# Performance work log

Measured on AMD Instinct MI355X. Metric: run time of the kernel, lower is better.

Reference implementation:

```python
import jax, jax.numpy as jnp
import numpy as np

N_NODES = 100000

def spmm(rows, cols, vals, x):
    # out[r] = sum_e vals[e] * x[cols[e]] for edges with rows[e] == r
    msgs = vals[:, None] * x[cols]            # [E, F]
    return jax.ops.segment_sum(msgs, rows, num_segments=N_NODES)

def setup_inputs() -> dict:
    key = jax.random.key(0)
    ks = jax.random.split(key, 8)
    N, E, F_IN, H, C = N_NODES, 1600000, 128, 128, 64
    x = jax.random.normal(ks[0], (N, F_IN), dtype=jnp.float32)
    edge_rows = jax.random.randint(ks[1], (E,), 0, N, dtype=jnp.int32)
    edge_cols = jax.random.randint(ks[2], (E,), 0, N, dtype=jnp.int32)
    edge_vals = jax.random.uniform(ks[3], (E,), dtype=jnp.float32)
    W1 = jax.random.normal(ks[4], (F_IN, H), dtype=jnp.float32) * (1.0 / np.sqrt(F_IN))
    b1 = jnp.zeros((H,), dtype=jnp.float32)
    W2 = jax.random.normal(ks[5], (H, C), dtype=jnp.float32) * (1.0 / np.sqrt(H))
    b2 = jnp.zeros((C,), dtype=jnp.float32)
    return {"x": x, "edge_rows": edge_rows, "edge_cols": edge_cols,
            "edge_vals": edge_vals, "W1": W1, "b1": b1, "W2": W2, "b2": b2}

def reference(x, edge_rows, edge_cols, edge_vals, W1, b1, W2, b2):
    # Layer 1: spmm(adj, x) then linear, then ReLU (dropout = identity at eval)
    h = spmm(edge_rows, edge_cols, edge_vals, x)   # [N, F_IN]
    h = h @ W1 + b1                                # [N, H]
    h = jax.nn.relu(h)
    # Layer 2
    h = spmm(edge_rows, edge_cols, edge_vals, h)   # [N, H]
    return h @ W2 + b2                             # [N, C]
```

## Files before the change

kernel.cpp:

```cpp
#include <hip/hip_runtime.h>


typedef __attribute__((ext_vector_type(8))) short short8;
typedef __attribute__((ext_vector_type(4))) float floatx4;
typedef __attribute__((ext_vector_type(2))) float floatx2;

#define ELLS 64
#define RW   256
#define CH   4096
#define EPT  16
#define MAXB 400

static __device__ __forceinline__ unsigned short f2bf(float f) {
    unsigned int u = __builtin_bit_cast(unsigned int, f);
    u += 0x7fffu + ((u >> 16) & 1u);
    return (unsigned short)(u >> 16);
}
static __device__ __forceinline__ float bflo(unsigned int u) {
    return __builtin_bit_cast(float, u << 16);
}
static __device__ __forceinline__ float bfhi(unsigned int u) {
    return __builtin_bit_cast(float, u & 0xffff0000u);
}
static __device__ __forceinline__ float slotval(unsigned int s) {
    return (float)(s >> 17) * (1.0f / 32767.0f);
}

__global__ __launch_bounds__(256) void prep_kernel(
    const float* __restrict__ W1, const float* __restrict__ W2,
    unsigned short* __restrict__ W1t, unsigned short* __restrict__ W2t)
{
    int idx = blockIdx.x * 256 + threadIdx.x;
    if (idx < 128 * 128) {
        int n = idx >> 7, k = idx & 127;
        W1t[idx] = f2bf(W1[(size_t)k * 128 + n]);
    }
    if (idx < 64 * 128) {
        int n = idx >> 7, k = idx & 127;
        W2t[idx] = f2bf(W2[(size_t)k * 64 + n]);
    }
}

static __device__ __forceinline__ void gemm1_body(
    const float* __restrict__ A, const unsigned short* __restrict__ Wt,
    unsigned short* __restrict__ Ys, int NP, int N, int bid)
{
    const int lane = threadIdx.x & 63;
    const int wave = threadIdx.x >> 6;
    const int quad = lane >> 4;
    const int l16  = lane & 15;
    const int row0 = bid * 64 + wave * 16;
    int arow = row0 + l16;
    if (arow > N - 1) arow = N - 1;

    short8 af[4];
    const float* ap = A + (size_t)arow * 128 + quad * 8;
    #pragma unroll
    for (int kt = 0; kt < 4; ++kt) {
        const floatx4* p = (const floatx4*)(ap + kt * 32);
        floatx4 lo = __builtin_nontemporal_load(p);
        floatx4 hi = __builtin_nontemporal_load(p + 1);
        short8 t;
        t[0] = (short)f2bf(lo[0]); t[1] = (short)f2bf(lo[1]);
        t[2] = (short)f2bf(lo[2]); t[3] = (short)f2bf(lo[3]);
        t[4] = (short)f2bf(hi[0]); t[5] = (short)f2bf(hi[1]);
        t[6] = (short)f2bf(hi[2]); t[7] = (short)f2bf(hi[3]);
        af[kt] = t;
    }

    floatx4 acc[8];
    #pragma unroll
    for (int nt = 0; nt < 8; ++nt) acc[nt] = (floatx4){0.f, 0.f, 0.f, 0.f};

    #pragma unroll
    for (int nt = 0; nt < 8; ++nt) {
        const unsigned short* wp = Wt + (size_t)(nt * 16 + l16) * 128 + quad * 8;
        #pragma unroll
        for (int kt = 0; kt < 4; ++kt) {
            short8 bfr = *(const short8*)(wp + kt * 32);
            acc[nt] = __builtin_amdgcn_mfma_f32_16x16x32_bf16(
                af[kt], bfr, acc[nt], 0, 0, 0);
        }
    }

    #pragma unroll
    for (int nt = 0; nt < 8; ++nt) {
        #pragma unroll
        for (int r = 0; r < 4; ++r) {
            int row = row0 + quad * 4 + r;
            if (row < N)
                Ys[(size_t)nt * NP * 16 + (size_t)row * 16 + l16] =
                    f2bf(acc[nt][r]);
        }
    }
}

__global__ __launch_bounds__(256) void binA_gemm1_fused(
    const int* __restrict__ erow, const int* __restrict__ ecol,
    const float* __restrict__ eval,
    uint2* __restrict__ slab, unsigned int* __restrict__ offsT,
    int E, int NC, int NB,
    const float* __restrict__ x, const unsigned short* __restrict__ W1t,
    unsigned short* __restrict__ y1s, int NP, int N)
{
    __shared__ unsigned int hist[MAXB + 1];
    __shared__ uint2 compact[CH];

    if ((int)blockIdx.x < NC) {
        const int t     = threadIdx.x;
        const int chunk = blockIdx.x;

        for (int i = t; i <= NB; i += 256) hist[i] = 0;
        __syncthreads();

        int base = chunk * CH + t * EPT;
        unsigned int w0[EPT];
        unsigned int vb[EPT];
        int bk[EPT], rk[EPT];

        if (base + EPT <= E) {
            #pragma unroll
            for (int q = 0; q < 4; ++q) {
                int4   r4 = *(const int4*)(erow + base + q * 4);
                int4   c4 = *(const int4*)(ecol + base + q * 4);
                float4 v4 = *(const float4*)(eval + base + q * 4);
                int rr[4]   = {r4.x, r4.y, r4.z, r4.w};
                int cc[4]   = {c4.x, c4.y, c4.z, c4.w};
                float vv[4] = {v4.x, v4.y, v4.z, v4.w};
                #pragma unroll
                for (int j = 0; j < 4; ++j) {
                    int i = q * 4 + j;
                    bk[i] = rr[j] >> 8;
                    w0[i] = (unsigned int)cc[j]
                          | (((unsigned int)rr[j] & (RW - 1)) << 17);
                    vb[i] = __builtin_bit_cast(unsigned int, vv[j]);
                }
            }
        } else {
            #pragma unroll
            for (int j = 0; j < EPT; ++j) {
                int e = base + j;
                if (e < E) {
                    int r = erow[e];
                    bk[j] = r >> 8;
                    w0[j] = (unsigned int)ecol[e]
                          | (((unsigned int)r & (RW - 1)) << 17);
                    vb[j] = __builtin_bit_cast(unsigned int, eval[e]);
                } else {
                    bk[j] = NB;
                    w0[j] = 0u; vb[j] = 0u;
                }
            }
        }

        #pragma unroll
        for (int j = 0; j < EPT; ++j)
            rk[j] = (int)atomicAdd(&hist[bk[j]], 1u);
        __syncthreads();

        if (t == 0) {
            unsigned int run = 0;
            for (int i = 0; i <= NB; ++i) {
                unsigned int c = hist[i];
                hist[i] = run;
                run += c;
            }
        }
        __syncthreads();

        #pragma unroll
        for (int j = 0; j < EPT; ++j) {
            unsigned int pos = hist[bk[j]] + (unsigned int)rk[j];
            uint2 e; e.x = w0[j]; e.y = vb[j];
            compact[pos] = e;
        }
        __syncthreads();

        uint2* sp = slab + (size_t)chunk * CH;
        #pragma unroll
        for (int s = 0; s < EPT; ++s)
            sp[s * 256 + t] = compact[s * 256 + t];
        unsigned int* op = offsT + (size_t)chunk * (NB + 1);
        for (int i = t; i <= NB; i += 256) op[i] = hist[i];
    } else {
        gemm1_body(x, W1t, y1s, NP, N, blockIdx.x - NC);
    }
}

__global__ __launch_bounds__(256) void binB(
    const uint2* __restrict__ slab, const unsigned int* __restrict__ offsT,
    unsigned int* __restrict__ ell, int* __restrict__ deg,
    int* __restrict__ dmax, int NC, int NB, int N)
{
    __shared__ unsigned int ell_lds[RW * ELLS];
    __shared__ unsigned int cur[RW];

    const int t = threadIdx.x;
    const int b = blockIdx.x;

    for (int i = t; i < RW; i += 256) cur[i] = 0;
    __syncthreads();

    const int grp = t >> 5;
    const int sl  = t & 31;
    for (int cbase = 0; cbase < NC; cbase += 8) {
        int c = cbase + grp;
        if (c < NC) {
            const unsigned int* op = offsT + (size_t)c * (NB + 1) + b;
            unsigned int off = op[0];
            unsigned int end = op[1];
            const uint2* sp = slab + (size_t)c * CH;
            for (unsigned int i = off + (unsigned)sl; i < end; i += 32) {
                uint2 e = sp[i];
                unsigned int rin = e.x >> 17;
                unsigned int col = e.x & 0x1FFFFu;
                float v = __builtin_bit_cast(float, e.y);
                unsigned int q = (unsigned int)(int)(v * 32767.f + 0.5f);
                unsigned int p = atomicAdd(&cur[rin], 1u);
                if (p < ELLS) {
                    unsigned int blk = ((p >> 2) + rin) & 15u;
                    ell_lds[rin * ELLS + blk * 4 + (p & 3)] = col | (q << 17);
                }
            }
        }
    }
    __syncthreads();

    uint4* dst = (uint4*)(ell + (size_t)b * RW * ELLS);
    const int s4 = t >> 4;
    const int r  = t & 15;
    #pragma unroll
    for (int s = 0; s < 16; ++s) {
        unsigned int sblk = (unsigned)((s4 + r) & 15);
        uint4 q = *(const uint4*)(ell_lds + ((s * 16 + r) * ELLS + sblk * 4));
        dst[s * 256 + s4 * 16 + r] = q;
    }

    int row = b * RW + t;
    if (row < N) deg[row] = min((int)cur[t], ELLS);
    if (t < 16) {
        int m = 0;
        #pragma unroll
        for (int i = 0; i < 16; ++i)
            m = max(m, (int)cur[t * 16 + i]);
        dmax[b * 16 + t] = min(m, ELLS);
    }
}

__global__ __launch_bounds__(256) void spmm1_sliced(
    const int* __restrict__ deg, const int* __restrict__ dmax,
    const unsigned int* __restrict__ ell,
    const unsigned short* __restrict__ y1s, const float* __restrict__ b1,
    unsigned short* __restrict__ h2s, int NP, int N)
{
    const int slice = blockIdx.x & 7;
    const int rblk  = blockIdx.x >> 3;
    const int wave  = threadIdx.x >> 6;
    const int lane  = threadIdx.x & 63;
    const int r     = lane >> 2;
    const int fl    = lane & 3;
    const int g     = rblk * 4 + wave;
    const int row   = g * 16 + r;

    int d  = (row < N) ? deg[row] : 0;
    int nb = (dmax[g] + 3) >> 2;

    const uint4* eg = (const uint4*)ell + (size_t)g * 256;
    const unsigned int* xu = (const unsigned int*)y1s + (size_t)slice * NP * 8;

    float a0 = 0.f, a1 = 0.f, a2 = 0.f, a3 = 0.f;
    for (int i4 = 0; i4 < nb; ++i4) {
        uint4 q = eg[i4 * 16 + r];
        unsigned int s[4] = {q.x, q.y, q.z, q.w};
        uint2 u[4];
        #pragma unroll
        for (int j = 0; j < 4; ++j) {
            s[j] = (i4 * 4 + j < d) ? s[j] : 0u;
            u[j] = *((const uint2*)(xu + (s[j] & 0x1FFFFu) * 8) + fl);
        }
        #pragma unroll
        for (int j = 0; j < 4; ++j) {
            float v = slotval(s[j]);
            a0 = fmaf(v, bflo(u[j].x), a0);
            a1 = fmaf(v, bfhi(u[j].x), a1);
            a2 = fmaf(v, bflo(u[j].y), a2);
            a3 = fmaf(v, bfhi(u[j].y), a3);
        }
    }

    if (row < N) {
        float4 b = ((const float4*)b1)[slice * 4 + fl];
        unsigned int p0 = (unsigned int)f2bf(fmaxf(a0 + b.x, 0.f))
                        | ((unsigned int)f2bf(fmaxf(a1 + b.y, 0.f)) << 16);
        unsigned int p1 = (unsigned int)f2bf(fmaxf(a2 + b.z, 0.f))
                        | ((unsigned int)f2bf(fmaxf(a3 + b.w, 0.f)) << 16);
        uint2 o; o.x = p0; o.y = p1;
        *(uint2*)((unsigned int*)h2s + (size_t)slice * NP * 8
                  + (size_t)row * 8 + fl * 2) = o;
    }
}

__global__ __launch_bounds__(256) void gemm2_kernel(
    const unsigned short* __restrict__ h2s,
    const unsigned short* __restrict__ W2t,
    unsigned short* __restrict__ y2s, int NP, int N)
{
    const int lane = threadIdx.x & 63;
    const int wave = threadIdx.x >> 6;
    const int quad = lane >> 4;
    const int l16  = lane & 15;
    const int row0 = blockIdx.x * 64 + wave * 16;
    int arow = row0 + l16;
    if (arow > N - 1) arow = N - 1;

    short8 af[4];
    #pragma unroll
    for (int kt = 0; kt < 4; ++kt) {
        int slice = kt * 2 + (quad >> 1);
        af[kt] = *(const short8*)(h2s + (size_t)slice * NP * 16
                                  + (size_t)arow * 16 + (quad & 1) * 8);
    }

    floatx4 acc[4];
    #pragma unroll
    for (int nt = 0; nt < 4; ++nt) acc[nt] = (floatx4){0.f, 0.f, 0.f, 0.f};

    #pragma unroll
    for (int nt = 0; nt < 4; ++nt) {
        const unsigned short* wp = W2t + (size_t)(nt * 16 + l16) * 128 + quad * 8;
        #pragma unroll
        for (int kt = 0; kt < 4; ++kt) {
            short8 bfr = *(const short8*)(wp + kt * 32);
            acc[nt] = __builtin_amdgcn_mfma_f32_16x16x32_bf16(
                af[kt], bfr, acc[nt], 0, 0, 0);
        }
    }

    #pragma unroll
    for (int nt = 0; nt < 4; ++nt) {
        #pragma unroll
        for (int r = 0; r < 4; ++r) {
            int row = row0 + quad * 4 + r;
            if (row < N)
                y2s[(size_t)nt * NP * 16 + (size_t)row * 16 + l16] =
                    f2bf(acc[nt][r]);
        }
    }
}

__global__ __launch_bounds__(256) void spmm2_sliced(
    const int* __restrict__ deg, const int* __restrict__ dmax,
    const unsigned int* __restrict__ ell,
    const unsigned short* __restrict__ y2s, const float* __restrict__ b2,
    float* __restrict__ out, int NP, int N)
{
    const int slice = blockIdx.x & 3;
    const int rblk  = blockIdx.x >> 2;
    const int wave  = threadIdx.x >> 6;
    const int lane  = threadIdx.x & 63;
    const int r     = lane >> 2;
    const int fl    = lane & 3;
    const int g     = rblk * 4 + wave;
    const int row   = g * 16 + r;

    int d  = (row < N) ? deg[row] : 0;
    int nb = (dmax[g] + 3) >> 2;

    const uint4* eg = (const uint4*)ell + (size_t)g * 256;
    const unsigned int* xu = (const unsigned int*)y2s + (size_t)slice * NP * 8;

    float a0 = 0.f, a1 = 0.f, a2 = 0.f, a3 = 0.f;
    for (int i4 = 0; i4 < nb; ++i4) {
        uint4 q = eg[i4 * 16 + r];
        unsigned int s[4] = {q.x, q.y, q.z, q.w};
        uint2 u[4];
        #pragma unroll
        for (int j = 0; j < 4; ++j) {
            s[j] = (i4 * 4 + j < d) ? s[j] : 0u;
            u[j] = *((const uint2*)(xu + (s[j] & 0x1FFFFu) * 8) + fl);
        }
        #pragma unroll
        for (int j = 0; j < 4; ++j) {
            float v = slotval(s[j]);
            a0 = fmaf(v, bflo(u[j].x), a0);
            a1 = fmaf(v, bfhi(u[j].x), a1);
            a2 = fmaf(v, bflo(u[j].y), a2);
            a3 = fmaf(v, bfhi(u[j].y), a3);
        }
    }

    if (row < N) {
        float4 b = ((const float4*)b2)[slice * 4 + fl];
        floatx4 o;
        o[0] = a0 + b.x; o[1] = a1 + b.y; o[2] = a2 + b.z; o[3] = a3 + b.w;
        __builtin_nontemporal_store(
            o, (floatx4*)(out + (size_t)row * 64 + slice * 16 + fl * 4));
    }
}

extern "C" void kernel_launch(void* const* d_in, const int* in_sizes, int n_in,
                              void* d_out, int out_size, void* d_ws, size_t ws_size,
                              hipStream_t stream)
{
    const float* x    = (const float*)d_in[0];
    const int*   erow = (const int*)  d_in[1];
    const int*   ecol = (const int*)  d_in[2];
    const float* eval = (const float*)d_in[3];
    const float* W1   = (const float*)d_in[4];
    const float* b1   = (const float*)d_in[5];
    const float* W2   = (const float*)d_in[6];
    const float* b2   = (const float*)d_in[7];
    float*       out  = (float*)d_out;

    const int N = in_sizes[0] / 128;
    const int E = in_sizes[1];
    const int NP = N + 128;
    const int NB = (N + RW - 1) / RW;
    const int NC = (E + CH - 1) / CH;

    unsigned short* y1s = (unsigned short*)d_ws;
    unsigned short* h2s = y1s + (size_t)NP * 128;
    unsigned short* W1t = h2s + (size_t)NP * 128;
    unsigned short* W2t = W1t + 128 * 128;
    unsigned int* ell   = (unsigned int*)(W2t + 64 * 128);
    uint2* slab         = (uint2*)(ell + (size_t)NB * RW * ELLS);
    unsigned int* offsT = (unsigned int*)(slab + (size_t)NC * CH);
    int* deg            = (int*)(offsT + (size_t)NC * (NB + 1));
    int* dmax           = deg + N;
    unsigned short* y2s = (unsigned short*)slab;

    const int mfma_blocks = (N + 63) / 64;
    const int prep_blocks = (128 * 128 + 255) / 256;
    const int rtiles      = (N + 63) / 64;
    const int s1_blocks   = rtiles * 8;
    const int s2_blocks   = rtiles * 4;

    prep_kernel<<<prep_blocks, 256, 0, stream>>>(W1, W2, W1t, W2t);

    binA_gemm1_fused<<<NC + mfma_blocks, 256, 0, stream>>>(
        erow, ecol, eval, slab, offsT, E, NC, NB, x, W1t, y1s, NP, N);

    binB<<<NB, 256, 0, stream>>>(slab, offsT, ell, deg, dmax, NC, NB, N);

    spmm1_sliced<<<s1_blocks, 256, 0, stream>>>(
        deg, dmax, ell, y1s, b1, h2s, NP, N);

    gemm2_kernel<<<mfma_blocks, 256, 0, stream>>>(h2s, W2t, y2s, NP, N);

    spmm2_sliced<<<s2_blocks, 256, 0, stream>>>(
        deg, dmax, ell, y2s, b2, out, NP, N);
}
```

Before: 316.7 us.

## Widen feature slices to 32 and zero-pad ELL instead of per-row degree masks

Feature slices for the intermediate bf16 matrices widen from 16 to 32 columns, so each lane in the SpMM kernels gathers 16 bytes (uint4) per neighbor and keeps eight accumulators. This halves the number of slice blocks and the number of times the ELL index lists are re-read. The ELL table is now zero-filled in LDS before binning, which lets the per-row degree array and the per-slot masking be dropped. Padded slots then contribute zero-valued gathers from row 0. The trade-off is more registers per lane and fewer blocks in flight, and the GEMM output and input layouts change to match.

```diff
diff --git a/kernel.cpp b/kernel.cpp
--- a/kernel.cpp
+++ b/kernel.cpp
@@ -3,7 +3,6 @@
 
 typedef __attribute__((ext_vector_type(8))) short short8;
 typedef __attribute__((ext_vector_type(4))) float floatx4;
-typedef __attribute__((ext_vector_type(2))) float floatx2;
 
 #define ELLS 64
 #define RW   256
@@ -89,8 +88,8 @@
         for (int r = 0; r < 4; ++r) {
             int row = row0 + quad * 4 + r;
             if (row < N)
-                Ys[(size_t)nt * NP * 16 + (size_t)row * 16 + l16] =
-                    f2bf(acc[nt][r]);
+                Ys[(size_t)(nt >> 1) * NP * 32 + (size_t)row * 32
+                   + (nt & 1) * 16 + l16] = f2bf(acc[nt][r]);
         }
     }
 }
@@ -189,8 +188,8 @@
 
 __global__ __launch_bounds__(256) void binB(
     const uint2* __restrict__ slab, const unsigned int* __restrict__ offsT,
-    unsigned int* __restrict__ ell, int* __restrict__ deg,
-    int* __restrict__ dmax, int NC, int NB, int N)
+    unsigned int* __restrict__ ell, int* __restrict__ dmax,
+    int NC, int NB, int N)
 {
     __shared__ unsigned int ell_lds[RW * ELLS];
     __shared__ unsigned int cur[RW];
@@ -198,6 +197,10 @@
     const int t = threadIdx.x;
     const int b = blockIdx.x;
 
+    uint4* z = (uint4*)ell_lds;
+    #pragma unroll
+    for (int i = 0; i < (RW * ELLS / 4) / 256; ++i)
+        z[i * 256 + t] = make_uint4(0u, 0u, 0u, 0u);
     for (int i = t; i < RW; i += 256) cur[i] = 0;
     __syncthreads();
 
@@ -236,8 +239,6 @@
         dst[s * 256 + s4 * 16 + r] = q;
     }
 
-    int row = b * RW + t;
-    if (row < N) deg[row] = min((int)cur[t], ELLS);
     if (t < 16) {
         int m = 0;
         #pragma unroll
@@ -248,111 +249,9 @@
 }
 
 __global__ __launch_bounds__(256) void spmm1_sliced(
-    const int* __restrict__ deg, const int* __restrict__ dmax,
-    const unsigned int* __restrict__ ell,
+    const int* __restrict__ dmax, const unsigned int* __restrict__ ell,
     const unsigned short* __restrict__ y1s, const float* __restrict__ b1,
     unsigned short* __restrict__ h2s, int NP, int N)
-{
-    const int slice = blockIdx.x & 7;
-    const int rblk  = blockIdx.x >> 3;
-    const int wave  = threadIdx.x >> 6;
-    const int lane  = threadIdx.x & 63;
-    const int r     = lane >> 2;
-    const int fl    = lane & 3;
-    const int g     = rblk * 4 + wave;
-    const int row   = g * 16 + r;
-
-    int d  = (row < N) ? deg[row] : 0;
-    int nb = (dmax[g] + 3) >> 2;
-
-    const uint4* eg = (const uint4*)ell + (size_t)g * 256;
-    const unsigned int* xu = (const unsigned int*)y1s + (size_t)slice * NP * 8;
-
-    float a0 = 0.f, a1 = 0.f, a2 = 0.f, a3 = 0.f;
-    for (int i4 = 0; i4 < nb; ++i4) {
-        uint4 q = eg[i4 * 16 + r];
-        unsigned int s[4] = {q.x, q.y, q.z, q.w};
-        uint2 u[4];
-        #pragma unroll
-        for (int j = 0; j < 4; ++j) {
-            s[j] = (i4 * 4 + j < d) ? s[j] : 0u;
-            u[j] = *((const uint2*)(xu + (s[j] & 0x1FFFFu) * 8) + fl);
-        }
-        #pragma unroll
-        for (int j = 0; j < 4; ++j) {
-            float v = slotval(s[j]);
-            a0 = fmaf(v, bflo(u[j].x), a0);
-            a1 = fmaf(v, bfhi(u[j].x), a1);
-            a2 = fmaf(v, bflo(u[j].y), a2);
-            a3 = fmaf(v, bfhi(u[j].y), a3);
-        }
-    }
-
-    if (row < N) {
-        float4 b = ((const float4*)b1)[slice * 4 + fl];
-        unsigned int p0 = (unsigned int)f2bf(fmaxf(a0 + b.x, 0.f))
-                        | ((unsigned int)f2bf(fmaxf(a1 + b.y, 0.f)) << 16);
-        unsigned int p1 = (unsigned int)f2bf(fmaxf(a2 + b.z, 0.f))
-                        | ((unsigned int)f2bf(fmaxf(a3 + b.w, 0.f)) << 16);
-        uint2 o; o.x = p0; o.y = p1;
-        *(uint2*)((unsigned int*)h2s + (size_t)slice * NP * 8
-                  + (size_t)row * 8 + fl * 2) = o;
-    }
-}
-
-__global__ __launch_bounds__(256) void gemm2_kernel(
-    const unsigned short* __restrict__ h2s,
-    const unsigned short* __restrict__ W2t,
-    unsigned short* __restrict__ y2s, int NP, int N)
-{
-    const int lane = threadIdx.x & 63;
-    const int wave = threadIdx.x >> 6;
-    const int quad = lane >> 4;
-    const int l16  = lane & 15;
-    const int row0 = blockIdx.x * 64 + wave * 16;
-    int arow = row0 + l16;
-    if (arow > N - 1) arow = N - 1;
-
-    short8 af[4];
-    #pragma unroll
-    for (int kt = 0; kt < 4; ++kt) {
-        int slice = kt * 2 + (quad >> 1);
-        af[kt] = *(const short8*)(h2s + (size_t)slice * NP * 16
-                                  + (size_t)arow * 16 + (quad & 1) * 8);
-    }
-
-    floatx4 acc[4];
-    #pragma unroll
-    for (int nt = 0; nt < 4; ++nt) acc[nt] = (floatx4){0.f, 0.f, 0.f, 0.f};
-
-    #pragma unroll
-    for (int nt = 0; nt < 4; ++nt) {
-        const unsigned short* wp = W2t + (size_t)(nt * 16 + l16) * 128 + quad * 8;
-        #pragma unroll
-        for (int kt = 0; kt < 4; ++kt) {
-            short8 bfr = *(const short8*)(wp + kt * 32);
-            acc[nt] = __builtin_amdgcn_mfma_f32_16x16x32_bf16(
-                af[kt], bfr, acc[nt], 0, 0, 0);
-        }
-    }
-
-    #pragma unroll
-    for (int nt = 0; nt < 4; ++nt) {
-        #pragma unroll
-        for (int r = 0; r < 4; ++r) {
-            int row = row0 + quad * 4 + r;
-            if (row < N)
-                y2s[(size_t)nt * NP * 16 + (size_t)row * 16 + l16] =
-                    f2bf(acc[nt][r]);
-        }
-    }
-}
-
-__global__ __launch_bounds__(256) void spmm2_sliced(
-    const int* __restrict__ deg, const int* __restrict__ dmax,
-    const unsigned int* __restrict__ ell,
-    const unsigned short* __restrict__ y2s, const float* __restrict__ b2,
-    float* __restrict__ out, int NP, int N)
 {
     const int slice = blockIdx.x & 3;
     const int rblk  = blockIdx.x >> 2;
@@ -363,38 +262,144 @@
     const int g     = rblk * 4 + wave;
     const int row   = g * 16 + r;
 
-    int d  = (row < N) ? deg[row] : 0;
     int nb = (dmax[g] + 3) >> 2;
 
     const uint4* eg = (const uint4*)ell + (size_t)g * 256;
-    const unsigned int* xu = (const unsigned int*)y2s + (size_t)slice * NP * 8;
+    const unsigned int* xu = (const unsigned int*)y1s + (size_t)slice * NP * 16;
 
     float a0 = 0.f, a1 = 0.f, a2 = 0.f, a3 = 0.f;
+    float a4 = 0.f, a5 = 0.f, a6 = 0.f, a7 = 0.f;
+
     for (int i4 = 0; i4 < nb; ++i4) {
         uint4 q = eg[i4 * 16 + r];
         unsigned int s[4] = {q.x, q.y, q.z, q.w};
-        uint2 u[4];
-        #pragma unroll
-        for (int j = 0; j < 4; ++j) {
-            s[j] = (i4 * 4 + j < d) ? s[j] : 0u;
-            u[j] = *((const uint2*)(xu + (s[j] & 0x1FFFFu) * 8) + fl);
-        }
+        uint4 u[4];
+        #pragma unroll
+        for (int j = 0; j < 4; ++j)
+            u[j] = *((const uint4*)(xu + (s[j] & 0x1FFFFu) * 16) + fl);
         #pragma unroll
         for (int j = 0; j < 4; ++j) {
             float v = slotval(s[j]);
-            a0 = fmaf(v, bflo(u[j].x), a0);
-            a1 = fmaf(v, bfhi(u[j].x), a1);
-            a2 = fmaf(v, bflo(u[j].y), a2);
-            a3 = fmaf(v, bfhi(u[j].y), a3);
+            a0 = fmaf(v, bflo(u[j].x), a0); a1 = fmaf(v, bfhi(u[j].x), a1);
+            a2 = fmaf(v, bflo(u[j].y), a2); a3 = fmaf(v, bfhi(u[j].y), a3);
+            a4 = fmaf(v, bflo(u[j].z), a4); a5 = fmaf(v, bfhi(u[j].z), a5);
+            a6 = fmaf(v, bflo(u[j].w), a6); a7 = fmaf(v, bfhi(u[j].w), a7);
         }
     }
 
     if (row < N) {
-        float4 b = ((const float4*)b2)[slice * 4 + fl];
-        floatx4 o;
-        o[0] = a0 + b.x; o[1] = a1 + b.y; o[2] = a2 + b.z; o[3] = a3 + b.w;
-        __builtin_nontemporal_store(
-            o, (floatx4*)(out + (size_t)row * 64 + slice * 16 + fl * 4));
+        const float4* bp = (const float4*)b1 + slice * 8 + fl * 2;
+        float4 bx = bp[0], by = bp[1];
+        uint4 o;
+        o.x = (unsigned int)f2bf(fmaxf(a0 + bx.x, 0.f))
+            | ((unsigned int)f2bf(fmaxf(a1 + bx.y, 0.f)) << 16);
+        o.y = (unsigned int)f2bf(fmaxf(a2 + bx.z, 0.f))
+            | ((unsigned int)f2bf(fmaxf(a3 + bx.w, 0.f)) << 16);
+        o.z = (unsigned int)f2bf(fmaxf(a4 + by.x, 0.f))
+            | ((unsigned int)f2bf(fmaxf(a5 + by.y, 0.f)) << 16);
+        o.w = (unsigned int)f2bf(fmaxf(a6 + by.z, 0.f))
+            | ((unsigned int)f2bf(fmaxf(a7 + by.w, 0.f)) << 16);
+        *(uint4*)((unsigned int*)h2s + (size_t)slice * NP * 16
+                  + (size_t)row * 16 + fl * 4) = o;
+    }
+}
+
+__global__ __launch_bounds__(256) void gemm2_kernel(
+    const unsigned short* __restrict__ h2s,
+    const unsigned short* __restrict__ W2t,
+    unsigned short* __restrict__ y2s, int NP, int N)
+{
+    const int lane = threadIdx.x & 63;
+    const int wave = threadIdx.x >> 6;
+    const int quad = lane >> 4;
+    const int l16  = lane & 15;
+    const int row0 = blockIdx.x * 64 + wave * 16;
+    int arow = row0 + l16;
+    if (arow > N - 1) arow = N - 1;
+
+    short8 af[4];
+    #pragma unroll
+    for (int kt = 0; kt < 4; ++kt)
+        af[kt] = *(const short8*)(h2s + (size_t)kt * NP * 32
+                                  + (size_t)arow * 32 + quad * 8);
+
+    floatx4 acc[4];
+    #pragma unroll
+    for (int nt = 0; nt < 4; ++nt) acc[nt] = (floatx4){0.f, 0.f, 0.f, 0.f};
+
+    #pragma unroll
+    for (int nt = 0; nt < 4; ++nt) {
+        const unsigned short* wp = W2t + (size_t)(nt * 16 + l16) * 128 + quad * 8;
+        #pragma unroll
+        for (int kt = 0; kt < 4; ++kt) {
+            short8 bfr = *(const short8*)(wp + kt * 32);
+            acc[nt] = __builtin_amdgcn_mfma_f32_16x16x32_bf16(
+                af[kt], bfr, acc[nt], 0, 0, 0);
+        }
+    }
+
+    #pragma unroll
+    for (int nt = 0; nt < 4; ++nt) {
+        #pragma unroll
+        for (int r = 0; r < 4; ++r) {
+            int row = row0 + quad * 4 + r;
+            if (row < N)
+                y2s[(size_t)(nt >> 1) * NP * 32 + (size_t)row * 32
+                    + (nt & 1) * 16 + l16] = f2bf(acc[nt][r]);
+        }
+    }
+}
+
+__global__ __launch_bounds__(256) void spmm2_sliced(
+    const int* __restrict__ dmax, const unsigned int* __restrict__ ell,
+    const unsigned short* __restrict__ y2s, const float* __restrict__ b2,
+    float* __restrict__ out, int NP, int N)
+{
+    const int slice = blockIdx.x & 1;
+    const int rblk  = blockIdx.x >> 1;
+    const int wave  = threadIdx.x >> 6;
+    const int lane  = threadIdx.x & 63;
+    const int r     = lane >> 2;
+    const int fl    = lane & 3;
+    const int g     = rblk * 4 + wave;
+    const int row   = g * 16 + r;
+
+    int nb = (dmax[g] + 3) >> 2;
+
+    const uint4* eg = (const uint4*)ell + (size_t)g * 256;
+    const unsigned int* xu = (const unsigned int*)y2s + (size_t)slice * NP * 16;
+
+    float a0 = 0.f, a1 = 0.f, a2 = 0.f, a3 = 0.f;
+    float a4 = 0.f, a5 = 0.f, a6 = 0.f, a7 = 0.f;
+
+    for (int i4 = 0; i4 < nb; ++i4) {
+        uint4 q = eg[i4 * 16 + r];
+        unsigned int s[4] = {q.x, q.y, q.z, q.w};
+        uint4 u[4];
+        #pragma unroll
+        for (int j = 0; j < 4; ++j)
+            u[j] = *((const uint4*)(xu + (s[j] & 0x1FFFFu) * 16) + fl);
+        #pragma unroll
+        for (int j = 0; j < 4; ++j) {
+            float v = slotval(s[j]);
+            a0 = fmaf(v, bflo(u[j].x), a0); a1 = fmaf(v, bfhi(u[j].x), a1);
+            a2 = fmaf(v, bflo(u[j].y), a2); a3 = fmaf(v, bfhi(u[j].y), a3);
+            a4 = fmaf(v, bflo(u[j].z), a4); a5 = fmaf(v, bfhi(u[j].z), a5);
+            a6 = fmaf(v, bflo(u[j].w), a6); a7 = fmaf(v, bfhi(u[j].w), a7);
+        }
+    }
+
+    if (row < N) {
+        const float4* bp = (const float4*)b2 + slice * 8 + fl * 2;
+        float4 bx = bp[0], by = bp[1];
+        float* op = out + (size_t)row * 64 + slice * 32 + fl * 8;
+        floatx4 o0, o1;
+        o0[0] = a0 + bx.x; o0[1] = a1 + bx.y;
+        o0[2] = a2 + bx.z; o0[3] = a3 + bx.w;
+        o1[0] = a4 + by.x; o1[1] = a5 + by.y;
+        o1[2] = a6 + by.z; o1[3] = a7 + by.w;
+        __builtin_nontemporal_store(o0, (floatx4*)op);
+        __builtin_nontemporal_store(o1, (floatx4*)(op + 4));
     }
 }
 
@@ -417,6 +422,7 @@
     const int NP = N + 128;
     const int NB = (N + RW - 1) / RW;
     const int NC = (E + CH - 1) / CH;
+    const int NGRP = NB * 16;
 
     unsigned short* y1s = (unsigned short*)d_ws;
     unsigned short* h2s = y1s + (size_t)NP * 128;
@@ -425,28 +431,27 @@
     unsigned int* ell   = (unsigned int*)(W2t + 64 * 128);
     uint2* slab         = (uint2*)(ell + (size_t)NB * RW * ELLS);
     unsigned int* offsT = (unsigned int*)(slab + (size_t)NC * CH);
-    int* deg            = (int*)(offsT + (size_t)NC * (NB + 1));
-    int* dmax           = deg + N;
+    int* dmax           = (int*)(offsT + (size_t)NC * (NB + 1));
     unsigned short* y2s = (unsigned short*)slab;
 
     const int mfma_blocks = (N + 63) / 64;
     const int prep_blocks = (128 * 128 + 255) / 256;
-    const int rtiles      = (N + 63) / 64;
-    const int s1_blocks   = rtiles * 8;
-    const int s2_blocks   = rtiles * 4;
+    const int gblk        = NGRP / 4;
+    const int s1_blocks   = gblk * 4;
+    const int s2_blocks   = gblk * 2;
 
     prep_kernel<<<prep_blocks, 256, 0, stream>>>(W1, W2, W1t, W2t);
 
     binA_gemm1_fused<<<NC + mfma_blocks, 256, 0, stream>>>(
         erow, ecol, eval, slab, offsT, E, NC, NB, x, W1t, y1s, NP, N);
 
-    binB<<<NB, 256, 0, stream>>>(slab, offsT, ell, deg, dmax, NC, NB, N);
+    binB<<<NB, 256, 0, stream>>>(slab, offsT, ell, dmax, NC, NB, N);
 
     spmm1_sliced<<<s1_blocks, 256, 0, stream>>>(
-        deg, dmax, ell, y1s, b1, h2s, NP, N);
+        dmax, ell, y1s, b1, h2s, NP, N);
 
     gemm2_kernel<<<mfma_blocks, 256, 0, stream>>>(h2s, W2t, y2s, NP, N);
 
     spmm2_sliced<<<s2_blocks, 256, 0, stream>>>(
-        deg, dmax, ell, y2s, b2, out, NP, N);
-}
+        dmax, ell, y2s, b2, out, NP, N);
+}
```

After: 294.1 us. -7.1%, faster.
